# Kernel optimization log

Hardware: AMD Instinct MI355X
Metric: run time of the kernel (lower is better)

The kernel has to match this reference:

```python
import jax, jax.numpy as jnp
import numpy as np
import math

D_MODEL, N_HEADS, D_FF = 1024, 16, 4096
D_K = D_MODEL // N_HEADS
B, S = 4, 2048
EPS = 1e-5


def layer_norm(x, gamma, beta):
    mean = jnp.mean(x, axis=-1, keepdims=True)
    var = jnp.mean((x - mean) ** 2, axis=-1, keepdims=True)  # unbiased=False
    return gamma * (x - mean) / jnp.sqrt(var + EPS) + beta


def setup_inputs() -> dict:
    key = jax.random.key(0)
    ks = jax.random.split(key, 7)
    std_attn = math.sqrt(2.0 / (D_MODEL + D_MODEL))
    std_ff1 = math.sqrt(2.0 / (D_MODEL + D_FF))
    std_ff2 = math.sqrt(2.0 / (D_FF + D_MODEL))
    return {
        "x": jax.random.normal(ks[0], (B, S, D_MODEL), jnp.float32),
        "W_q": jax.random.normal(ks[1], (D_MODEL, D_MODEL), jnp.float32) * std_attn,
        "W_k": jax.random.normal(ks[2], (D_MODEL, D_MODEL), jnp.float32) * std_attn,
        "W_v": jax.random.normal(ks[3], (D_MODEL, D_MODEL), jnp.float32) * std_attn,
        "W_o": jax.random.normal(ks[4], (D_MODEL, D_MODEL), jnp.float32) * std_attn,
        "W1": jax.random.normal(ks[5], (D_MODEL, D_FF), jnp.float32) * std_ff1,
        "b1": jnp.zeros((D_FF,), jnp.float32),
        "W2": jax.random.normal(ks[6], (D_FF, D_MODEL), jnp.float32) * std_ff2,
        "b2": jnp.zeros((D_MODEL,), jnp.float32),
        "ln1_gamma": jnp.ones((D_MODEL,), jnp.float32),
        "ln1_beta": jnp.zeros((D_MODEL,), jnp.float32),
        "ln2_gamma": jnp.ones((D_MODEL,), jnp.float32),
        "ln2_beta": jnp.zeros((D_MODEL,), jnp.float32),
    }


def reference(x, W_q, W_k, W_v, W_o, W1, b1, W2, b2,
              ln1_gamma, ln1_beta, ln2_gamma, ln2_beta):
    b, s, d = x.shape
    # pre-LN attention block
    ln1 = layer_norm(x, ln1_gamma, ln1_beta)
    q = (ln1 @ W_q).reshape(b, s, N_HEADS, D_K)
    k = (ln1 @ W_k).reshape(b, s, N_HEADS, D_K)
    v = (ln1 @ W_v).reshape(b, s, N_HEADS, D_K)
    scores = jnp.einsum("bqhd,bkhd->bhqk", q, k) / math.sqrt(D_K)
    attn = jax.nn.softmax(scores, axis=-1)
    ctx = jnp.einsum("bhqk,bkhd->bqhd", attn, v).reshape(b, s, d)
    attn_out = ctx @ W_o
    attn_residual = x + attn_out
    # pre-LN FFN block
    ln2 = layer_norm(attn_residual, ln2_gamma, ln2_beta)
    ff = jax.nn.relu(ln2 @ W1 + b1) @ W2 + b2
    return attn_residual + ff
```

## Files before the change

### kernel.cpp

```cpp
#include <hip/hip_runtime.h>
#include <hip/hip_bf16.h>

typedef __attribute__((ext_vector_type(4)))  float  floatx4;
typedef __attribute__((ext_vector_type(16))) float  floatx16;
typedef __attribute__((ext_vector_type(8)))  short  shortx8;
typedef __attribute__((ext_vector_type(4)))  short  shortx4;

__device__ __forceinline__ short f2bf(float f) {
    unsigned u = __float_as_uint(f);
    u += 0x7fffu + ((u >> 16) & 1u);
    return (short)(u >> 16);
}
__device__ __forceinline__ float bf2f(short s) {
    return __uint_as_float(((unsigned)(unsigned short)s) << 16);
}
__device__ __forceinline__ float fast_exp2(float x) {
#if __has_builtin(__builtin_amdgcn_exp2f)
    return __builtin_amdgcn_exp2f(x);
#else
    return exp2f(x);
#endif
}

__device__ __forceinline__ void load_lds16(const void* g, void* l) {
    __builtin_amdgcn_global_load_lds(
        (const __attribute__((address_space(1))) unsigned int*)g,
        (__attribute__((address_space(3))) unsigned int*)l,
        16, 0, 0);
}

__global__ __launch_bounds__(256)
void transpose_w(const float* __restrict__ src, short* __restrict__ dst, int K, int N)
{
    __shared__ __align__(16) float tile[32][33];
    const int n0 = blockIdx.x * 32, k0 = blockIdx.y * 32;
    const int tx = threadIdx.x & 31, ty = threadIdx.x >> 5;
    for (int i = 0; i < 32; i += 8)
        tile[ty + i][tx] = src[(size_t)(k0 + ty + i) * N + n0 + tx];
    __syncthreads();
    for (int i = 0; i < 32; i += 8)
        dst[(size_t)(n0 + ty + i) * K + k0 + tx] = f2bf(tile[tx][ty + i]);
}

__global__ __launch_bounds__(256)
void ln_bf16(const float* __restrict__ x, const float* __restrict__ g,
             const float* __restrict__ be, short* __restrict__ out)
{
    const int row = blockIdx.x;
    const int tid = threadIdx.x;
    const float4 v = reinterpret_cast<const float4*>(x + (size_t)row * 1024)[tid];
    float s  = v.x + v.y + v.z + v.w;
    float ss = v.x * v.x + v.y * v.y + v.z * v.z + v.w * v.w;
    for (int off = 32; off > 0; off >>= 1) {
        s  += __shfl_down(s,  off);
        ss += __shfl_down(ss, off);
    }
    __shared__ float rs[4], rss[4];
    const int wave = tid >> 6, lane = tid & 63;
    if (lane == 0) { rs[wave] = s; rss[wave] = ss; }
    __syncthreads();
    const float S    = rs[0] + rs[1] + rs[2] + rs[3];
    const float SS   = rss[0] + rss[1] + rss[2] + rss[3];
    const float mean = S * (1.0f / 1024.0f);
    const float var  = SS * (1.0f / 1024.0f) - mean * mean;
    const float rstd = rsqrtf(var + 1e-5f);
    const float4 gg = reinterpret_cast<const float4*>(g)[tid];
    const float4 bb = reinterpret_cast<const float4*>(be)[tid];
    shortx4 o;
    o[0] = f2bf(gg.x * ((v.x - mean) * rstd) + bb.x);
    o[1] = f2bf(gg.y * ((v.y - mean) * rstd) + bb.y);
    o[2] = f2bf(gg.z * ((v.z - mean) * rstd) + bb.z);
    o[3] = f2bf(gg.w * ((v.w - mean) * rstd) + bb.w);
    *reinterpret_cast<shortx4*>(out + (size_t)row * 1024 + tid * 4) = o;
}

__device__ __forceinline__ floatx4 mfma2(shortx8 a0, shortx8 a1,
                                         shortx8 b0, shortx8 b1, floatx4 c) {
    c = __builtin_amdgcn_mfma_f32_16x16x32_bf16(a0, b0, c, 0, 0, 0);
    return __builtin_amdgcn_mfma_f32_16x16x32_bf16(a1, b1, c, 0, 0, 0);
}

template <int EPI>
__global__ __launch_bounds__(512, 2)
void gemm256(const short* __restrict__ A, const short* __restrict__ Bt,
             short* __restrict__ Cb, float* __restrict__ Cf,
             const float* __restrict__ bias, const float* __restrict__ resid,
             int M, int N, int K, int tilesN, int nsplit)
{
    extern __shared__ __align__(16) short lds[];
    short* const As0 = lds;
    short* const Bs0 = lds + 16384;
    short* const As1 = lds + 32768;
    short* const Bs1 = lds + 49152;

    int wg = blockIdx.x;
    {
        const int nwg = gridDim.x;
        const int q = nwg >> 3, r = nwg & 7;
        const int xcd = wg & 7, loc = wg >> 3;
        wg = (xcd < r ? xcd * (q + 1) : r * (q + 1) + (xcd - r) * q) + loc;
    }
    const int ntiles = gridDim.x / nsplit;
    const int sp   = wg / ntiles;
    const int tile = wg - sp * ntiles;
    const int tm = tile / tilesN, tn = tile - tm * tilesN;
    const size_t bm = (size_t)tm * 256, bn = (size_t)tn * 256;
    const int Ks   = K / nsplit;
    const int kbeg = sp * Ks;

    const int tid  = threadIdx.x;
    const int wave = tid >> 6;
    const int lane = tid & 63;
    const int quad = lane >> 4;
    const int l16  = lane & 15;
    const int wm   = wave >> 2;
    const int wn   = wave & 3;

    const int x7  = l16 & 7;
    const int go0 = ((quad    ) ^ x7) * 8;
    const int go1 = ((quad + 4) ^ x7) * 8;
    const int aoff = (wm * 128 + l16) * 64;
    const int boff = (wn *  64 + l16) * 64;

    const int rcall = tid >> 3;
    const int gl    = (tid & 7) ^ (rcall & 7);
    const short* srcA = A  + (bm + rcall) * (size_t)K + kbeg + gl * 8;
    const short* srcB = Bt + (bn + rcall) * (size_t)K + kbeg + gl * 8;
    const int dstw = wave * 512;

#define STG(dst, src, c, k0) \
    load_lds16((src) + (size_t)(c) * 64 * K + (k0), (dst) + (c) * 4096 + dstw)

    const int NT = Ks >> 6;

    STG(As0, srcA, 0, 0); STG(As0, srcA, 2, 0);
    STG(Bs0, srcB, 0, 0); STG(Bs0, srcB, 1, 0);
    STG(Bs0, srcB, 2, 0); STG(Bs0, srcB, 3, 0);
    STG(As0, srcA, 1, 0); STG(As0, srcA, 3, 0);

    floatx4 acc[8][4];
#pragma unroll
    for (int i = 0; i < 8; i++)
#pragma unroll
        for (int j = 0; j < 4; j++)
            acc[i][j] = (floatx4){0.f, 0.f, 0.f, 0.f};

    asm volatile("s_waitcnt vmcnt(2)" ::: "memory");
    __builtin_amdgcn_s_barrier();

#define GTILE(AsR, BsR, AsW, BsW, kw, dopf)                                   \
  do {                                                                        \
    shortx8 aF[4][2], bF[2][2];                                               \
    _Pragma("unroll") for (int mi = 0; mi < 4; ++mi) {                        \
        aF[mi][0] = *(const shortx8*)&AsR[aoff + mi * 1024 + go0];            \
        aF[mi][1] = *(const shortx8*)&AsR[aoff + mi * 1024 + go1];            \
    }                                                                         \
    _Pragma("unroll") for (int ni = 0; ni < 2; ++ni) {                        \
        bF[ni][0] = *(const shortx8*)&BsR[boff + ni * 1024 + go0];            \
        bF[ni][1] = *(const shortx8*)&BsR[boff + ni * 1024 + go1];            \
    }                                                                         \
    if (dopf) { STG(AsW, srcA, 0, kw); STG(AsW, srcA, 2, kw); }               \
    __builtin_amdgcn_s_barrier();                                             \
    asm volatile("s_waitcnt lgkmcnt(0)" ::: "memory");                        \
    __builtin_amdgcn_s_setprio(1);                                            \
    _Pragma("unroll") for (int mi = 0; mi < 4; ++mi)                          \
        _Pragma("unroll") for (int ni = 0; ni < 2; ++ni)                      \
            acc[mi][ni] = mfma2(aF[mi][0], aF[mi][1], bF[ni][0], bF[ni][1],   \
                                acc[mi][ni]);                                 \
    __builtin_amdgcn_s_setprio(0);                                            \
    __builtin_amdgcn_s_barrier();                                             \
    _Pragma("unroll") for (int ni = 0; ni < 2; ++ni) {                        \
        bF[ni][0] = *(const shortx8*)&BsR[boff + (ni + 2) * 1024 + go0];      \
        bF[ni][1] = *(const shortx8*)&BsR[boff + (ni + 2) * 1024 + go1];      \
    }                                                                         \
    if (dopf) { STG(BsW, srcB, 0, kw); STG(BsW, srcB, 1, kw); }               \
    __builtin_amdgcn_s_barrier();                                             \
    asm volatile("s_waitcnt lgkmcnt(0)" ::: "memory");                        \
    __builtin_amdgcn_s_setprio(1);                                            \
    _Pragma("unroll") for (int mi = 0; mi < 4; ++mi)                          \
        _Pragma("unroll") for (int ni = 0; ni < 2; ++ni)                      \
            acc[mi][ni + 2] = mfma2(aF[mi][0], aF[mi][1], bF[ni][0],          \
                                    bF[ni][1], acc[mi][ni + 2]);              \
    __builtin_amdgcn_s_setprio(0);                                            \
    if (dopf) asm volatile("s_waitcnt vmcnt(4)" ::: "memory");                \
    else      asm volatile("s_waitcnt vmcnt(0)" ::: "memory");                \
    __builtin_amdgcn_s_barrier();                                             \
    _Pragma("unroll") for (int mi = 0; mi < 4; ++mi) {                        \
        aF[mi][0] = *(const shortx8*)&AsR[aoff + (mi + 4) * 1024 + go0];      \
        aF[mi][1] = *(const shortx8*)&AsR[aoff + (mi + 4) * 1024 + go1];      \
    }                                                                         \
    if (dopf) { STG(BsW, srcB, 2, kw); STG(BsW, srcB, 3, kw); }               \
    __builtin_amdgcn_s_barrier();                                             \
    asm volatile("s_waitcnt lgkmcnt(0)" ::: "memory");                        \
    __builtin_amdgcn_s_setprio(1);                                            \
    _Pragma("unroll") for (int mi = 0; mi < 4; ++mi)                          \
        _Pragma("unroll") for (int ni = 0; ni < 2; ++ni)                      \
            acc[mi + 4][ni + 2] = mfma2(aF[mi][0], aF[mi][1], bF[ni][0],      \
                                        bF[ni][1], acc[mi + 4][ni + 2]);      \
    __builtin_amdgcn_s_setprio(0);                                            \
    __builtin_amdgcn_s_barrier();                                             \
    _Pragma("unroll") for (int ni = 0; ni < 2; ++ni) {                        \
        bF[ni][0] = *(const shortx8*)&BsR[boff + ni * 1024 + go0];            \
        bF[ni][1] = *(const shortx8*)&BsR[boff + ni * 1024 + go1];            \
    }                                                                         \
    if (dopf) { STG(AsW, srcA, 1, kw); STG(AsW, srcA, 3, kw); }               \
    __builtin_amdgcn_s_barrier();                                             \
    asm volatile("s_waitcnt lgkmcnt(0)" ::: "memory");                        \
    __builtin_amdgcn_s_setprio(1);                                            \
    _Pragma("unroll") for (int mi = 0; mi < 4; ++mi)                          \
        _Pragma("unroll") for (int ni = 0; ni < 2; ++ni)                      \
            acc[mi + 4][ni] = mfma2(aF[mi][0], aF[mi][1], bF[ni][0],          \
                                    bF[ni][1], acc[mi + 4][ni]);              \
    __builtin_amdgcn_s_setprio(0);                                            \
    if (dopf) asm volatile("s_waitcnt vmcnt(2)" ::: "memory");                \
    __builtin_amdgcn_s_barrier();                                             \
  } while (0)

    const int NH = NT >> 1;
    for (int u = 0; u < NH; ++u) {
        GTILE(As0, Bs0, As1, Bs1, ((2 * u + 1) << 6), true);
        const bool pf2 = (u + 1) < NH;
        GTILE(As1, Bs1, As0, Bs0, ((2 * u + 2) << 6), pf2);
    }
#undef GTILE
#undef STG

#pragma unroll
    for (int mi = 0; mi < 8; ++mi) {
#pragma unroll
        for (int ni = 0; ni < 4; ++ni) {
            const size_t row0 = bm + wm * 128 + mi * 16 + quad * 4;
            const size_t col  = bn + wn * 64 + ni * 16 + l16;
#pragma unroll
            for (int r = 0; r < 4; ++r) {
                float v = acc[mi][ni][r];
                const size_t idx = (row0 + r) * (size_t)N + col;
                if (EPI == 0) {
                    Cb[idx] = f2bf(v);
                } else if (EPI == 1) {
                    v += bias[col];
                    Cb[idx] = f2bf(v > 0.f ? v : 0.f);
                } else if (EPI == 2) {
                    Cf[idx] = resid[idx] + v;
                } else if (EPI == 3) {
                    v += bias[col];
                    Cf[idx] = resid[idx] + v;
                } else {
                    if (sp == 0) v += bias[col];
                    atomicAdd(&Cf[idx], v);
                }
            }
        }
    }
}

__global__ __launch_bounds__(256)
void transpose_v(const short* __restrict__ qkv, short* __restrict__ vt)
{
    __shared__ __align__(16) short tile[64][65];
    const int st = blockIdx.x, h = blockIdx.y, b = blockIdx.z;
    const int t = threadIdx.x;
    for (int i = 0; i < 2; i++) {
        const int idx = i * 256 + t;
        const int s = idx >> 3, dg = idx & 7;
        shortx8 val = *(const shortx8*)&qkv[(size_t)(b * 2048 + st * 64 + s) * 3072
                                           + 2048 + h * 64 + dg * 8];
        for (int u = 0; u < 8; u++) tile[s][dg * 8 + u] = val[u];
    }
    __syncthreads();
    const int d = t >> 2, sg = (t & 3) * 16;
    shortx8 lo, hi;
    for (int i = 0; i < 8; i++) {
        lo[i] = tile[sg + i][d];
        hi[i] = tile[sg + 8 + i][d];
    }
    const size_t base = ((size_t)(b * 16 + h) * 64 + d) * 2048 + st * 64 + sg;
    *(shortx8*)&vt[base]     = lo;
    *(shortx8*)&vt[base + 8] = hi;
}

__global__ __launch_bounds__(512, 4)
void attention_kernel(const short* __restrict__ qkv, const short* __restrict__ vt,
                      short* __restrict__ ctx)
{
    const int qt = blockIdx.x, h = blockIdx.y, b = blockIdx.z;
    const int tid  = threadIdx.x;
    const int wave = tid >> 6;
    const int lane = tid & 63;
    const int l32  = lane & 31;
    const int hf   = lane >> 5;

    __shared__ __align__(16) short Ks[64 * 72];
    __shared__ __align__(16) short Vs[64 * 72];
    __shared__ __align__(16) short Ps[8][32 * 72];

    const int q0 = qt * 256 + wave * 32;
    const float qscale = 0.125f * 1.44269504088896f;
    const short* qrow = qkv + (size_t)(b * 2048 + q0 + l32) * 3072 + h * 64;
    shortx8 qf[4];
    for (int dk = 0; dk < 4; dk++) {
        shortx8 raw = *(const shortx8*)&qrow[dk * 16 + hf * 8];
        for (int j = 0; j < 8; j++) raw[j] = f2bf(bf2f(raw[j]) * qscale);
        qf[dk] = raw;
    }

    floatx16 accO[2];
    for (int t = 0; t < 2; t++)
        for (int r = 0; r < 16; r++) accO[t][r] = 0.f;
    float lsum = 0.f;

    const short* kbase = qkv + (size_t)(b * 2048) * 3072 + 1024 + h * 64;
    const short* vbase = vt + ((size_t)(b * 16 + h) * 64) * 2048;
    short* const psw = &Ps[wave][0];
    unsigned* const pswd = (unsigned*)psw;

    const int ss = tid >> 3, sdg = tid & 7;

    for (int kt = 0; kt < 32; ++kt) {
        __syncthreads();
        {
            shortx8 kv = *(const shortx8*)&kbase[(size_t)(kt * 64 + ss) * 3072 + sdg * 8];
            *(shortx8*)&Ks[ss * 72 + sdg * 8] = kv;
            shortx8 vv = *(const shortx8*)&vbase[(size_t)ss * 2048 + kt * 64 + sdg * 8];
            *(shortx8*)&Vs[ss * 72 + sdg * 8] = vv;
        }
        __syncthreads();

        for (int t = 0; t < 2; t++) {
            floatx16 c;
            for (int r = 0; r < 16; r++) c[r] = 0.f;
            for (int dk = 0; dk < 4; dk++) {
                shortx8 kf = *(const shortx8*)&Ks[(t * 32 + l32) * 72 + dk * 16 + hf * 8];
                c = __builtin_amdgcn_mfma_f32_32x32x16_bf16(kf, qf[dk], c, 0, 0, 0);
            }
            for (int R = 0; R < 4; R++) {
                float2 a, bb;
                a.x  = fast_exp2(c[4 * R + 0]);
                a.y  = fast_exp2(c[4 * R + 1]);
                bb.x = fast_exp2(c[4 * R + 2]);
                bb.y = fast_exp2(c[4 * R + 3]);
                lsum += (a.x + a.y) + (bb.x + bb.y);
                union { __hip_bfloat162 h2[2]; uint2 u; } pk;
                pk.h2[0] = __float22bfloat162_rn(a);
                pk.h2[1] = __float22bfloat162_rn(bb);
                *(uint2*)&pswd[l32 * 36 + t * 16 + 4 * R + 2 * hf] = pk.u;
            }
        }
        asm volatile("s_waitcnt lgkmcnt(0)" ::: "memory");

        shortx8 pf[4];
        for (int sk = 0; sk < 4; sk++)
            pf[sk] = *(const shortx8*)&psw[l32 * 72 + sk * 16 + hf * 8];

        for (int t = 0; t < 2; t++) {
            floatx16 c = accO[t];
            for (int sk = 0; sk < 4; sk++) {
                shortx8 vf = *(const shortx8*)&Vs[(t * 32 + l32) * 72 + sk * 16 + hf * 8];
                c = __builtin_amdgcn_mfma_f32_32x32x16_bf16(vf, pf[sk], c, 0, 0, 0);
            }
            accO[t] = c;
        }
    }

    const float lfull = lsum + __shfl_xor(lsum, 32);
    const float inv = 1.0f / lfull;
    const size_t crow = (size_t)(b * 2048 + q0 + l32) * 1024 + h * 64;
    for (int t = 0; t < 2; t++)
        for (int R = 0; R < 4; R++) {
            float2 a, bb;
            a.x  = accO[t][4 * R + 0] * inv;
            a.y  = accO[t][4 * R + 1] * inv;
            bb.x = accO[t][4 * R + 2] * inv;
            bb.y = accO[t][4 * R + 3] * inv;
            union { __hip_bfloat162 h2[2]; uint2 u; } pk;
            pk.h2[0] = __float22bfloat162_rn(a);
            pk.h2[1] = __float22bfloat162_rn(bb);
            *(uint2*)&ctx[crow + t * 32 + 8 * R + 4 * hf] = pk.u;
        }
}

extern "C" void kernel_launch(void* const* d_in, const int* in_sizes, int n_in,
                              void* d_out, int out_size, void* d_ws, size_t ws_size,
                              hipStream_t stream)
{
    const float* x   = (const float*)d_in[0];
    const float* Wq  = (const float*)d_in[1];
    const float* Wk  = (const float*)d_in[2];
    const float* Wv  = (const float*)d_in[3];
    const float* Wo  = (const float*)d_in[4];
    const float* W1  = (const float*)d_in[5];
    const float* b1  = (const float*)d_in[6];
    const float* W2  = (const float*)d_in[7];
    const float* b2  = (const float*)d_in[8];
    const float* g1  = (const float*)d_in[9];
    const float* be1 = (const float*)d_in[10];
    const float* g2  = (const float*)d_in[11];
    const float* be2 = (const float*)d_in[12];
    float* out = (float*)d_out;
    char*  ws  = (char*)d_ws;

    const size_t MiB = 1u << 20;
    short* regA   = (short*)(ws);
    short* qkv    = (short*)(ws + 16 * MiB);
    short* vt     = (short*)(ws + 64 * MiB);
    short* ff1    = qkv;
    short* Wqkv_t = (short*)(ws + 80 * MiB);
    short* Wo_t   = (short*)(ws + 86 * MiB);
    short* W1_t   = (short*)(ws + 88 * MiB);
    short* W2_t   = (short*)(ws + 96 * MiB);

    const dim3 blk(256);
    const unsigned LDSB = 131072;

    static int attr_once = []() {
        hipFuncSetAttribute(reinterpret_cast<const void*>(gemm256<0>),
                            hipFuncAttributeMaxDynamicSharedMemorySize, 131072);
        hipFuncSetAttribute(reinterpret_cast<const void*>(gemm256<1>),
                            hipFuncAttributeMaxDynamicSharedMemorySize, 131072);
        hipFuncSetAttribute(reinterpret_cast<const void*>(gemm256<2>),
                            hipFuncAttributeMaxDynamicSharedMemorySize, 131072);
        hipFuncSetAttribute(reinterpret_cast<const void*>(gemm256<4>),
                            hipFuncAttributeMaxDynamicSharedMemorySize, 131072);
        return 0;
    }();
    (void)attr_once;

    transpose_w<<<dim3(32, 32),  blk, 0, stream>>>(Wq, Wqkv_t,                  1024, 1024);
    transpose_w<<<dim3(32, 32),  blk, 0, stream>>>(Wk, Wqkv_t + 1024 * 1024,    1024, 1024);
    transpose_w<<<dim3(32, 32),  blk, 0, stream>>>(Wv, Wqkv_t + 2 * 1024 * 1024,1024, 1024);
    transpose_w<<<dim3(32, 32),  blk, 0, stream>>>(Wo, Wo_t,                    1024, 1024);
    transpose_w<<<dim3(128, 32), blk, 0, stream>>>(W1, W1_t,                    1024, 4096);
    transpose_w<<<dim3(32, 128), blk, 0, stream>>>(W2, W2_t,                    4096, 1024);

    ln_bf16<<<8192, blk, 0, stream>>>(x, g1, be1, regA);
    gemm256<0><<<dim3(384), dim3(512), LDSB, stream>>>(regA, Wqkv_t, qkv, nullptr,
                                                       nullptr, nullptr, 8192, 3072, 1024, 12, 1);
    transpose_v<<<dim3(32, 16, 4), blk, 0, stream>>>(qkv, vt);
    attention_kernel<<<dim3(8, 16, 4), dim3(512), 0, stream>>>(qkv, vt, regA);
    gemm256<2><<<dim3(128), dim3(512), LDSB, stream>>>(regA, Wo_t, nullptr, out,
                                                       nullptr, x, 8192, 1024, 1024, 4, 1);
    ln_bf16<<<8192, blk, 0, stream>>>(out, g2, be2, regA);
    gemm256<1><<<dim3(512), dim3(512), LDSB, stream>>>(regA, W1_t, ff1, nullptr,
                                                       b1, nullptr, 8192, 4096, 1024, 16, 1);
    gemm256<4><<<dim3(256), dim3(512), LDSB, stream>>>(ff1, W2_t, nullptr, out,
                                                       b2, nullptr, 8192, 1024, 4096, 4, 2);
}
```

Baseline: 542.5 us.

## Replace ping-pong K64 GEMM mainloop with 4-stage K32 ring-buffer pipeline

Rewrites the GEMM main loop. The old version used two LDS buffers, each holding a 64-wide K tile, with hand-interleaved sub-phases and many barriers. The new version uses a 4-slot ring of 32-wide K tiles: it prefetches two tiles ahead, waits on vmcnt, issues one barrier per tile, and then loads all fragments and runs 32 MFMAs. This changes the LDS layout and swizzle and is meant to cut barrier count and deepen load latency hiding. The trade-offs are lost setprio/phase interleaving and a possible LDS race, since only one barrier per iteration guards slot reuse with a prefetch distance of 2 in 4 slots.

```diff
diff --git a/kernel.cpp b/kernel.cpp
--- a/kernel.cpp
+++ b/kernel.cpp
@@ -74,12 +74,6 @@
     *reinterpret_cast<shortx4*>(out + (size_t)row * 1024 + tid * 4) = o;
 }
 
-__device__ __forceinline__ floatx4 mfma2(shortx8 a0, shortx8 a1,
-                                         shortx8 b0, shortx8 b1, floatx4 c) {
-    c = __builtin_amdgcn_mfma_f32_16x16x32_bf16(a0, b0, c, 0, 0, 0);
-    return __builtin_amdgcn_mfma_f32_16x16x32_bf16(a1, b1, c, 0, 0, 0);
-}
-
 template <int EPI>
 __global__ __launch_bounds__(512, 2)
 void gemm256(const short* __restrict__ A, const short* __restrict__ Bt,
@@ -88,10 +82,6 @@
              int M, int N, int K, int tilesN, int nsplit)
 {
     extern __shared__ __align__(16) short lds[];
-    short* const As0 = lds;
-    short* const Bs0 = lds + 16384;
-    short* const As1 = lds + 32768;
-    short* const Bs1 = lds + 49152;
 
     int wg = blockIdx.x;
     {
@@ -116,27 +106,26 @@
     const int wm   = wave >> 2;
     const int wn   = wave & 3;
 
-    const int x7  = l16 & 7;
-    const int go0 = ((quad    ) ^ x7) * 8;
-    const int go1 = ((quad + 4) ^ x7) * 8;
-    const int aoff = (wm * 128 + l16) * 64;
-    const int boff = (wn *  64 + l16) * 64;
-
-    const int rcall = tid >> 3;
-    const int gl    = (tid & 7) ^ (rcall & 7);
+    const int swz  = (quad ^ ((l16 >> 1) & 3)) * 8;
+    const int abase = wm * 4096 + l16 * 32 + swz;
+    const int bbase = (wn >> 1) * 4096 + (wn & 1) * 2048 + l16 * 32 + swz;
+
+    const int rcall = tid >> 2;
+    const int gl    = (tid & 3) ^ ((rcall >> 1) & 3);
     const short* srcA = A  + (bm + rcall) * (size_t)K + kbeg + gl * 8;
     const short* srcB = Bt + (bn + rcall) * (size_t)K + kbeg + gl * 8;
     const int dstw = wave * 512;
 
-#define STG(dst, src, c, k0) \
-    load_lds16((src) + (size_t)(c) * 64 * K + (k0), (dst) + (c) * 4096 + dstw)
-
-    const int NT = Ks >> 6;
-
-    STG(As0, srcA, 0, 0); STG(As0, srcA, 2, 0);
-    STG(Bs0, srcB, 0, 0); STG(Bs0, srcB, 1, 0);
-    STG(Bs0, srcB, 2, 0); STG(Bs0, srcB, 3, 0);
-    STG(As0, srcA, 1, 0); STG(As0, srcA, 3, 0);
+    const int NT = Ks >> 5;
+
+#define STGT(j) do {                                                   \
+    short* bufp = lds + ((j) & 3) * 16384;                             \
+    const int kk = (j) << 5;                                           \
+    load_lds16(srcA + kk,                     bufp +         dstw);    \
+    load_lds16(srcA + (size_t)128 * K + kk,   bufp +  4096 + dstw);    \
+    load_lds16(srcB + kk,                     bufp +  8192 + dstw);    \
+    load_lds16(srcB + (size_t)128 * K + kk,   bufp + 12288 + dstw);    \
+  } while (0)
 
     floatx4 acc[8][4];
 #pragma unroll
@@ -145,85 +134,37 @@
         for (int j = 0; j < 4; j++)
             acc[i][j] = (floatx4){0.f, 0.f, 0.f, 0.f};
 
-    asm volatile("s_waitcnt vmcnt(2)" ::: "memory");
-    __builtin_amdgcn_s_barrier();
-
-#define GTILE(AsR, BsR, AsW, BsW, kw, dopf)                                   \
-  do {                                                                        \
-    shortx8 aF[4][2], bF[2][2];                                               \
-    _Pragma("unroll") for (int mi = 0; mi < 4; ++mi) {                        \
-        aF[mi][0] = *(const shortx8*)&AsR[aoff + mi * 1024 + go0];            \
-        aF[mi][1] = *(const shortx8*)&AsR[aoff + mi * 1024 + go1];            \
-    }                                                                         \
-    _Pragma("unroll") for (int ni = 0; ni < 2; ++ni) {                        \
-        bF[ni][0] = *(const shortx8*)&BsR[boff + ni * 1024 + go0];            \
-        bF[ni][1] = *(const shortx8*)&BsR[boff + ni * 1024 + go1];            \
-    }                                                                         \
-    if (dopf) { STG(AsW, srcA, 0, kw); STG(AsW, srcA, 2, kw); }               \
-    __builtin_amdgcn_s_barrier();                                             \
-    asm volatile("s_waitcnt lgkmcnt(0)" ::: "memory");                        \
-    __builtin_amdgcn_s_setprio(1);                                            \
-    _Pragma("unroll") for (int mi = 0; mi < 4; ++mi)                          \
-        _Pragma("unroll") for (int ni = 0; ni < 2; ++ni)                      \
-            acc[mi][ni] = mfma2(aF[mi][0], aF[mi][1], bF[ni][0], bF[ni][1],   \
-                                acc[mi][ni]);                                 \
-    __builtin_amdgcn_s_setprio(0);                                            \
-    __builtin_amdgcn_s_barrier();                                             \
-    _Pragma("unroll") for (int ni = 0; ni < 2; ++ni) {                        \
-        bF[ni][0] = *(const shortx8*)&BsR[boff + (ni + 2) * 1024 + go0];      \
-        bF[ni][1] = *(const shortx8*)&BsR[boff + (ni + 2) * 1024 + go1];      \
-    }                                                                         \
-    if (dopf) { STG(BsW, srcB, 0, kw); STG(BsW, srcB, 1, kw); }               \
-    __builtin_amdgcn_s_barrier();                                             \
-    asm volatile("s_waitcnt lgkmcnt(0)" ::: "memory");                        \
-    __builtin_amdgcn_s_setprio(1);                                            \
-    _Pragma("unroll") for (int mi = 0; mi < 4; ++mi)                          \
-        _Pragma("unroll") for (int ni = 0; ni < 2; ++ni)                      \
-            acc[mi][ni + 2] = mfma2(aF[mi][0], aF[mi][1], bF[ni][0],          \
-                                    bF[ni][1], acc[mi][ni + 2]);              \
-    __builtin_amdgcn_s_setprio(0);                                            \
-    if (dopf) asm volatile("s_waitcnt vmcnt(4)" ::: "memory");                \
-    else      asm volatile("s_waitcnt vmcnt(0)" ::: "memory");                \
-    __builtin_amdgcn_s_barrier();                                             \
-    _Pragma("unroll") for (int mi = 0; mi < 4; ++mi) {                        \
-        aF[mi][0] = *(const shortx8*)&AsR[aoff + (mi + 4) * 1024 + go0];      \
-        aF[mi][1] = *(const shortx8*)&AsR[aoff + (mi + 4) * 1024 + go1];      \
-    }                                                                         \
-    if (dopf) { STG(BsW, srcB, 2, kw); STG(BsW, srcB, 3, kw); }               \
-    __builtin_amdgcn_s_barrier();                                             \
-    asm volatile("s_waitcnt lgkmcnt(0)" ::: "memory");                        \
-    __builtin_amdgcn_s_setprio(1);                                            \
-    _Pragma("unroll") for (int mi = 0; mi < 4; ++mi)                          \
-        _Pragma("unroll") for (int ni = 0; ni < 2; ++ni)                      \
-            acc[mi + 4][ni + 2] = mfma2(aF[mi][0], aF[mi][1], bF[ni][0],      \
-                                        bF[ni][1], acc[mi + 4][ni + 2]);      \
-    __builtin_amdgcn_s_setprio(0);                                            \
-    __builtin_amdgcn_s_barrier();                                             \
-    _Pragma("unroll") for (int ni = 0; ni < 2; ++ni) {                        \
-        bF[ni][0] = *(const shortx8*)&BsR[boff + ni * 1024 + go0];            \
-        bF[ni][1] = *(const shortx8*)&BsR[boff + ni * 1024 + go1];            \
-    }                                                                         \
-    if (dopf) { STG(AsW, srcA, 1, kw); STG(AsW, srcA, 3, kw); }               \
-    __builtin_amdgcn_s_barrier();                                             \
-    asm volatile("s_waitcnt lgkmcnt(0)" ::: "memory");                        \
-    __builtin_amdgcn_s_setprio(1);                                            \
-    _Pragma("unroll") for (int mi = 0; mi < 4; ++mi)                          \
-        _Pragma("unroll") for (int ni = 0; ni < 2; ++ni)                      \
-            acc[mi + 4][ni] = mfma2(aF[mi][0], aF[mi][1], bF[ni][0],          \
-                                    bF[ni][1], acc[mi + 4][ni]);              \
-    __builtin_amdgcn_s_setprio(0);                                            \
-    if (dopf) asm volatile("s_waitcnt vmcnt(2)" ::: "memory");                \
-    __builtin_amdgcn_s_barrier();                                             \
-  } while (0)
-
-    const int NH = NT >> 1;
-    for (int u = 0; u < NH; ++u) {
-        GTILE(As0, Bs0, As1, Bs1, ((2 * u + 1) << 6), true);
-        const bool pf2 = (u + 1) < NH;
-        GTILE(As1, Bs1, As0, Bs0, ((2 * u + 2) << 6), pf2);
-    }
-#undef GTILE
-#undef STG
+    STGT(0);
+    STGT(1);
+
+    for (int t = 0; t < NT; ++t) {
+        if (t + 2 < NT) {
+            STGT(t + 2);
+            asm volatile("s_waitcnt vmcnt(8)" ::: "memory");
+        } else if (t + 1 < NT) {
+            asm volatile("s_waitcnt vmcnt(4)" ::: "memory");
+        } else {
+            asm volatile("s_waitcnt vmcnt(0)" ::: "memory");
+        }
+        __builtin_amdgcn_s_barrier();
+        asm volatile("" ::: "memory");
+
+        const short* bufc = lds + (t & 3) * 16384;
+        shortx8 aF[8], bF[4];
+#pragma unroll
+        for (int mi = 0; mi < 8; ++mi)
+            aF[mi] = *(const shortx8*)&bufc[abase + mi * 512];
+#pragma unroll
+        for (int ni = 0; ni < 4; ++ni)
+            bF[ni] = *(const shortx8*)&bufc[8192 + bbase + ni * 512];
+#pragma unroll
+        for (int mi = 0; mi < 8; ++mi)
+#pragma unroll
+            for (int ni = 0; ni < 4; ++ni)
+                acc[mi][ni] = __builtin_amdgcn_mfma_f32_16x16x32_bf16(
+                    aF[mi], bF[ni], acc[mi][ni], 0, 0, 0);
+    }
+#undef STGT
 
 #pragma unroll
     for (int mi = 0; mi < 8; ++mi) {
```

Measured after the change: 563.2 us. 1.04x slower.
